# Optimization experiments

Measured on AMD Instinct MI355X. Metric: run time of the kernel, lower is better.

## Reference

```python
import jax, jax.numpy as jnp
import numpy as np

POOL = 4      # pool_size
SR = 2        # sampling_ratio (fixed; torchvision adaptive default approximated)
C_IN = 1024
C1, C2 = 256, 128
OUT_DIM = 2048


def setup_inputs() -> dict:
    key = jax.random.key(0)
    ks = jax.random.split(key, 10)
    B, C, H, W = 8, C_IN, 64, 64
    N = 64
    x = jax.random.normal(ks[0], (B, C, H, W), dtype=jnp.float32)
    # boxes in image pixel coords (image is H*16 = 1024 px)
    img = 1024.0
    x1 = jax.random.uniform(ks[1], (B, N), minval=0.0, maxval=img - 260.0)
    y1 = jax.random.uniform(ks[2], (B, N), minval=0.0, maxval=img - 260.0)
    bw = jax.random.uniform(ks[3], (B, N), minval=32.0, maxval=256.0)
    bh = jax.random.uniform(ks[4], (B, N), minval=32.0, maxval=256.0)
    boxes = jnp.stack([x1, y1, x1 + bw, y1 + bh], axis=-1)  # [B,N,4]
    scale = jnp.float32(1.0 / 16.0)
    # detector params
    w1 = jax.random.normal(ks[5], (C1, C_IN), dtype=jnp.float32) / np.sqrt(C_IN)
    b1 = jnp.zeros((C1,), dtype=jnp.float32)
    w2 = jax.random.normal(ks[6], (C2, C1), dtype=jnp.float32) / np.sqrt(C1)
    b2 = jnp.zeros((C2,), dtype=jnp.float32)
    wl = jax.random.normal(ks[7], (OUT_DIM, C2 * POOL * POOL), dtype=jnp.float32) / np.sqrt(C2 * POOL * POOL)
    bl = jnp.zeros((OUT_DIM,), dtype=jnp.float32)
    return {"x": x, "boxes": boxes, "scale": scale,
            "w1": w1, "b1": b1, "w2": w2, "b2": b2, "wl": wl, "bl": bl}


def _axis_coords(start, size, H):
    # start,size: [R]; returns coords [R, POOL*SR], valid mask, int low/high, lerp wts
    bin_sz = size / POOL                       # [R]
    j = jnp.arange(POOL * SR, dtype=jnp.float32)
    off = jnp.floor(j / SR) + ((j % SR) + 0.5) / SR   # [P]
    c = start[:, None] + off[None, :] * bin_sz[:, None]  # [R,P]
    valid = (c >= -1.0) & (c <= H)
    c = jnp.clip(c, 0.0, H - 1.0)
    lo = jnp.floor(c).astype(jnp.int32)
    lo = jnp.minimum(lo, H - 1)
    hi = jnp.minimum(lo + 1, H - 1)
    frac = c - lo.astype(c.dtype)
    return valid, lo, hi, frac


def _roi_align(feat, boxes, scale):
    # feat: [B,C,H,W], boxes: [B,N,4] -> pooled [B*N, C, POOL, POOL]
    B, C, H, W = feat.shape
    N = boxes.shape[1]
    R = B * N
    bx = (boxes.reshape(R, 4) * scale)
    x1, y1, x2, y2 = bx[:, 0], bx[:, 1], bx[:, 2], bx[:, 3]
    rw = jnp.maximum(x2 - x1, 1.0)
    rh = jnp.maximum(y2 - y1, 1.0)
    vy, y_lo, y_hi, ly = _axis_coords(y1, rh, H)   # [R,P]
    vx, x_lo, x_hi, lx = _axis_coords(x1, rw, W)
    hy, hx = 1.0 - ly, 1.0 - lx
    bidx = jnp.repeat(jnp.arange(B, dtype=jnp.int32), N)  # [R]
    b = bidx[:, None, None]
    # gather 4 corners -> [R,P,P,C]
    v00 = feat[b, :, y_lo[:, :, None], x_lo[:, None, :]]
    v01 = feat[b, :, y_lo[:, :, None], x_hi[:, None, :]]
    v10 = feat[b, :, y_hi[:, :, None], x_lo[:, None, :]]
    v11 = feat[b, :, y_hi[:, :, None], x_hi[:, None, :]]
    w00 = (hy[:, :, None] * hx[:, None, :])[..., None]
    w01 = (hy[:, :, None] * lx[:, None, :])[..., None]
    w10 = (ly[:, :, None] * hx[:, None, :])[..., None]
    w11 = (ly[:, :, None] * lx[:, None, :])[..., None]
    val = v00 * w00 + v01 * w01 + v10 * w10 + v11 * w11
    mask = (vy[:, :, None] & vx[:, None, :])[..., None]
    val = jnp.where(mask, val, 0.0)            # [R,P,P,C]
    val = val.reshape(R, POOL, SR, POOL, SR, C).mean(axis=(2, 4))  # [R,POOL,POOL,C]
    return jnp.transpose(val, (0, 3, 1, 2))    # [R,C,POOL,POOL]


def reference(x, boxes, scale, w1, b1, w2, b2, wl, bl):
    pooled = _roi_align(x, boxes, scale)                  # [R,C,4,4]
    h = jax.nn.elu(jnp.einsum('rchw,oc->rohw', pooled, w1) + b1[None, :, None, None])
    h = jax.nn.elu(jnp.einsum('rchw,oc->rohw', h, w2) + b2[None, :, None, None])
    h = h.reshape(h.shape[0], -1)                         # [R, 128*16], torch Flatten order
    out = jax.nn.elu(h @ wl.T + bl)                       # [R, 2048]
    return out
```

## Files before the change

kernel.cpp:

```cpp
#include <hip/hip_runtime.h>
#include <math.h>

#define C_INK   1024
#define C1D     256
#define C2D     128
#define OUTD    2048
#define R_ROI   512
#define MPIX    32768

#define NSIDE   128

typedef _Float16 half8 __attribute__((ext_vector_type(8)));
typedef float    f32x4 __attribute__((ext_vector_type(4)));

__device__ __forceinline__ unsigned int pack2h(float a, float b) {
    union { _Float16 h[2]; unsigned int u; } p;
    p.h[0] = (_Float16)a; p.h[1] = (_Float16)b;
    return p.u;
}
__device__ __forceinline__ float eluf(float v) { return v > 0.f ? v : expf(v) - 1.f; }

template<int RC>
__device__ __forceinline__ half8* ldsq(_Float16* base, int row, int ch) {
    return reinterpret_cast<half8*>(base) + row * RC + (ch ^ (row & 7));
}

__global__ __launch_bounds__(256) void cvt_w1(
    const float* __restrict__ w1, _Float16* __restrict__ w1h)
{
    const int i0 = (blockIdx.x * 256 + threadIdx.x) * 4;
    #pragma unroll
    for (int j = 0; j < 4; ++j) {
        const int i = (i0 + j) * 4;
        const float4 v = *reinterpret_cast<const float4*>(w1 + i);
        uint2 u; u.x = pack2h(v.x, v.y); u.y = pack2h(v.z, v.w);
        *reinterpret_cast<uint2*>(w1h + i) = u;
    }
}

__global__ __launch_bounds__(512, 4) void conv1x1_f16(
    const float* __restrict__ x, const _Float16* __restrict__ w1h,
    const float* __restrict__ w2, const float* __restrict__ wl,
    _Float16* __restrict__ w2h, _Float16* __restrict__ wlh,
    _Float16* __restrict__ z)
{
    const int bid = blockIdx.x;
    const int tid = threadIdx.x;

    if (bid < NSIDE) {
        constexpr int NF4_W2 = (C2D * C1D) / 4;
        constexpr int NF4    = NF4_W2 + (OUTD * OUTD) / 4;
        for (int i = bid * 512 + tid; i < NF4; i += NSIDE * 512) {
            const float* s; _Float16* d; int e;
            if (i < NF4_W2) { s = w2; d = w2h; e = i * 4; }
            else            { s = wl; d = wlh; e = (i - NF4_W2) * 4; }
            const float4 v = *reinterpret_cast<const float4*>(s + e);
            uint2 u; u.x = pack2h(v.x, v.y); u.y = pack2h(v.z, v.w);
            *reinterpret_cast<uint2*>(d + e) = u;
        }
        return;
    }

    __shared__ __align__(16) _Float16 As[2][64 * 64];

    const int lane = tid & 63;
    const int wave = tid >> 6;
    const int m0   = (bid - NSIDE) * 64;
    const int b    = m0 >> 12;
    const int p0   = m0 & 4095;

    const float* xbase = x + (size_t)b * C_INK * 4096 + p0 + lane;
    const _Float16* wbase = w1h + (size_t)(wave * 32 + (lane & 15)) * C_INK + (lane >> 4) * 8;

    float ar_a[8], ar_b[8];
    half8 bf_a[2][2], bf_b[2][2];
    f32x4 acc[4][2];
    #pragma unroll
    for (int i = 0; i < 4; ++i)
        #pragma unroll
        for (int j = 0; j < 2; ++j) acc[i][j] = (f32x4){0.f, 0.f, 0.f, 0.f};

    auto LOADA = [&](float (&ar)[8], int k0) {
        const float* xk = xbase + (size_t)(k0 + wave * 8) * 4096;
        #pragma unroll
        for (int j = 0; j < 8; ++j) ar[j] = xk[(size_t)j * 4096];
    };
    auto LOADB = [&](half8 (&bf)[2][2], int k0) {
        #pragma unroll
        for (int kk = 0; kk < 2; ++kk)
            #pragma unroll
            for (int ni = 0; ni < 2; ++ni)
                bf[kk][ni] = *reinterpret_cast<const half8*>(
                    wbase + (size_t)ni * 16 * C_INK + k0 + kk * 32);
    };
    auto WRITEA = [&](int buf, float (&ar)[8]) {
        union { half8 h; unsigned int u[4]; } pk;
        #pragma unroll
        for (int j = 0; j < 4; ++j) pk.u[j] = pack2h(ar[2 * j], ar[2 * j + 1]);
        *ldsq<8>(&As[buf][0], lane, wave) = pk.h;
    };
    auto COMPUTE = [&](int buf, half8 (&bf)[2][2]) {
        #pragma unroll
        for (int kk = 0; kk < 2; ++kk) {
            const int ch = kk * 4 + (lane >> 4);
            half8 af[4];
            #pragma unroll
            for (int mi = 0; mi < 4; ++mi)
                af[mi] = *ldsq<8>(&As[buf][0], mi * 16 + (lane & 15), ch);
            #pragma unroll
            for (int mi = 0; mi < 4; ++mi)
                #pragma unroll
                for (int ni = 0; ni < 2; ++ni)
                    acc[mi][ni] = __builtin_amdgcn_mfma_f32_16x16x32_f16(bf[kk][ni], af[mi], acc[mi][ni], 0, 0, 0);
        }
    };

    LOADA(ar_a, 0);   LOADB(bf_a, 0);
    LOADA(ar_b, 64);  LOADB(bf_b, 64);
    WRITEA(0, ar_a);
    __syncthreads();

    #pragma unroll
    for (int tp = 0; tp < 8; ++tp) {
        const int t = 2 * tp;
        if (tp < 7) LOADA(ar_a, (t + 2) * 64);
        WRITEA(1, ar_b);
        COMPUTE(0, bf_a);
        if (tp < 7) LOADB(bf_a, (t + 2) * 64);
        __syncthreads();
        if (tp < 7) {
            LOADA(ar_b, (t + 3) * 64);
            WRITEA(0, ar_a);
        }
        COMPUTE(1, bf_b);
        if (tp < 7) LOADB(bf_b, (t + 3) * 64);
        __syncthreads();
    }

    _Float16* zp = z + (size_t)m0 * C1D;
    #pragma unroll
    for (int mi = 0; mi < 4; ++mi) {
        const int pixel = mi * 16 + (lane & 15);
        #pragma unroll
        for (int ni = 0; ni < 2; ++ni) {
            const int oc0 = wave * 32 + ni * 16 + (lane >> 4) * 4;
            uint2 u;
            u.x = pack2h(acc[mi][ni][0], acc[mi][ni][1]);
            u.y = pack2h(acc[mi][ni][2], acc[mi][ni][3]);
            *reinterpret_cast<uint2*>(&zp[(size_t)pixel * C1D + oc0]) = u;
        }
    }
}

__global__ __launch_bounds__(512) void roi_gemm2_f16(
    const _Float16* __restrict__ z, const float* __restrict__ boxes,
    const float* __restrict__ scale_p, const float* __restrict__ b1v,
    const _Float16* __restrict__ w2h, const float* __restrict__ b2v,
    _Float16* __restrict__ h2)
{
    __shared__ __align__(16) _Float16 H1s[16 * 256];
    __shared__ int   s_off[64][4];
    __shared__ float s_w[64][4];

    const int bid  = blockIdx.x;
    const int r    = (bid & 7) * 64 + (bid >> 3);
    const int tid  = threadIdx.x;
    const int lane = tid & 63;
    const int wv   = tid >> 6;

    half8 bfr[8];
    {
        const _Float16* wp = w2h + (size_t)(wv * 16 + (lane & 15)) * C1D + (lane >> 4) * 8;
        #pragma unroll
        for (int ks = 0; ks < 8; ++ks)
            bfr[ks] = *reinterpret_cast<const half8*>(wp + ks * 32);
    }

    if (tid < 64) {
        const float sc = scale_p[0];
        const float x1 = boxes[r * 4 + 0] * sc, y1 = boxes[r * 4 + 1] * sc;
        const float x2 = boxes[r * 4 + 2] * sc, y2 = boxes[r * 4 + 3] * sc;
        const float rw = fmaxf(x2 - x1, 1.f), rh = fmaxf(y2 - y1, 1.f);
        const int jy = tid >> 3, jx = tid & 7;

        float offy = (float)(jy >> 1) + (float)(jy & 1) * 0.5f + 0.25f;
        float cy = y1 + offy * rh * 0.25f;
        const bool vy = (cy >= -1.f) && (cy <= 64.f);
        cy = fminf(fmaxf(cy, 0.f), 63.f);
        int ylo = (int)cy; if (ylo > 63) ylo = 63;
        int yhi = ylo + 1; if (yhi > 63) yhi = 63;
        const float ly = cy - (float)ylo, hy = 1.f - ly;

        float offx = (float)(jx >> 1) + (float)(jx & 1) * 0.5f + 0.25f;
        float cx = x1 + offx * rw * 0.25f;
        const bool vx = (cx >= -1.f) && (cx <= 64.f);
        cx = fminf(fmaxf(cx, 0.f), 63.f);
        int xlo = (int)cx; if (xlo > 63) xlo = 63;
        int xhi = xlo + 1; if (xhi > 63) xhi = 63;
        const float lx = cx - (float)xlo, hx = 1.f - lx;

        const float wm = (vy && vx) ? 0.25f : 0.f;
        s_w[tid][0] = hy * hx * wm;
        s_w[tid][1] = hy * lx * wm;
        s_w[tid][2] = ly * hx * wm;
        s_w[tid][3] = ly * lx * wm;
        s_off[tid][0] = (ylo * 64 + xlo) * C1D;
        s_off[tid][1] = (ylo * 64 + xhi) * C1D;
        s_off[tid][2] = (yhi * 64 + xlo) * C1D;
        s_off[tid][3] = (yhi * 64 + xhi) * C1D;
    }
    __syncthreads();

    {
        const int ch8  = tid & 31;
        const int cell = tid >> 5;
        const _Float16* zb = z + (size_t)(r >> 6) * 4096 * C1D + ch8 * 8;

        float accv[8];
        #pragma unroll
        for (int e = 0; e < 8; ++e) accv[e] = 0.f;

        const int py = cell >> 2, px = cell & 3;
        #pragma unroll
        for (int u = 0; u < 4; ++u) {
            const int s = (py * 2 + (u >> 1)) * 8 + px * 2 + (u & 1);
            #pragma unroll
            for (int k = 0; k < 4; ++k) {
                const half8 v = *reinterpret_cast<const half8*>(zb + s_off[s][k]);
                const float w = s_w[s][k];
                #pragma unroll
                for (int e = 0; e < 8; ++e) accv[e] += (float)v[e] * w;
            }
        }

        const float4 b0 = *reinterpret_cast<const float4*>(&b1v[ch8 * 8]);
        const float4 b4 = *reinterpret_cast<const float4*>(&b1v[ch8 * 8 + 4]);
        half8 o;
        o[0] = (_Float16)eluf(accv[0] + b0.x); o[1] = (_Float16)eluf(accv[1] + b0.y);
        o[2] = (_Float16)eluf(accv[2] + b0.z); o[3] = (_Float16)eluf(accv[3] + b0.w);
        o[4] = (_Float16)eluf(accv[4] + b4.x); o[5] = (_Float16)eluf(accv[5] + b4.y);
        o[6] = (_Float16)eluf(accv[6] + b4.z); o[7] = (_Float16)eluf(accv[7] + b4.w);
        *ldsq<32>(H1s, cell, ch8) = o;
    }
    __syncthreads();

    f32x4 oa = (f32x4){0.f, 0.f, 0.f, 0.f};
    #pragma unroll
    for (int ks = 0; ks < 8; ++ks) {
        const int ch = ks * 4 + (lane >> 4);
        const half8 af = *ldsq<32>(H1s, lane & 15, ch);
        oa = __builtin_amdgcn_mfma_f32_16x16x32_f16(af, bfr[ks], oa, 0, 0, 0);
    }

    {
        const int o  = wv * 16 + (lane & 15);
        const int p0 = (lane >> 4) * 4;
        const float bv = b2v[o];
        uint2 u;
        u.x = pack2h(eluf(oa[0] + bv), eluf(oa[1] + bv));
        u.y = pack2h(eluf(oa[2] + bv), eluf(oa[3] + bv));
        *reinterpret_cast<uint2*>(&h2[(size_t)r * 2048 + o * 16 + p0]) = u;
    }
}

__global__ __launch_bounds__(512) void gemm_nt_out(
    const _Float16* __restrict__ A, const _Float16* __restrict__ W,
    const float* __restrict__ bias, float* __restrict__ Cout)
{
    constexpr int K = OUTD, N = OUTD;
    __shared__ __align__(16) _Float16 As[64 * 128];
    __shared__ __align__(16) _Float16 Bs[64 * 128];

    const int bid  = blockIdx.x;
    const int m0   = (bid >> 5) * 64;
    const int n0   = (bid & 31) * 64;

    const int tid  = threadIdx.x;
    const int lane = tid & 63;
    const int wave = tid >> 6;
    const int wr   = wave >> 2, wc = wave & 3;
    const int c    = tid & 7;
    const int r0   = tid >> 3;

    half8 arg[2], brg[2];
    f32x4 acc[2];
    acc[0] = (f32x4){0.f, 0.f, 0.f, 0.f};
    acc[1] = (f32x4){0.f, 0.f, 0.f, 0.f};

    auto LOADT = [&](int k0) {
        const _Float16* ap = &A[(size_t)(m0 + r0) * K + k0 + c * 16];
        arg[0] = *reinterpret_cast<const half8*>(ap);
        arg[1] = *reinterpret_cast<const half8*>(ap + 8);
        const _Float16* wp = &W[(size_t)(n0 + r0) * K + k0 + c * 16];
        brg[0] = *reinterpret_cast<const half8*>(wp);
        brg[1] = *reinterpret_cast<const half8*>(wp + 8);
    };
    auto WRITET = [&]() {
        *ldsq<16>(As, r0, 2 * c)     = arg[0];
        *ldsq<16>(As, r0, 2 * c + 1) = arg[1];
        *ldsq<16>(Bs, r0, 2 * c)     = brg[0];
        *ldsq<16>(Bs, r0, 2 * c + 1) = brg[1];
    };
    auto COMPUTET = [&]() {
        #pragma unroll
        for (int kk = 0; kk < 4; ++kk) {
            const int ch = kk * 4 + (lane >> 4);
            half8 af[2], bf;
            af[0] = *ldsq<16>(As, wr * 32 + (lane & 15), ch);
            af[1] = *ldsq<16>(As, wr * 32 + 16 + (lane & 15), ch);
            bf    = *ldsq<16>(Bs, wc * 16 + (lane & 15), ch);
            acc[0] = __builtin_amdgcn_mfma_f32_16x16x32_f16(bf, af[0], acc[0], 0, 0, 0);
            acc[1] = __builtin_amdgcn_mfma_f32_16x16x32_f16(bf, af[1], acc[1], 0, 0, 0);
        }
    };

    constexpr int nt = K / 128;
    LOADT(0); WRITET(); __syncthreads();
    for (int t = 0; t < nt - 1; ++t) {
        LOADT((t + 1) * 128);
        COMPUTET();
        __syncthreads();
        WRITET();
        __syncthreads();
    }
    COMPUTET();

    #pragma unroll
    for (int mi = 0; mi < 2; ++mi) {
        const int row  = m0 + wr * 32 + mi * 16 + (lane & 15);
        const int col0 = n0 + wc * 16 + (lane >> 4) * 4;
        const float4 bv = *reinterpret_cast<const float4*>(&bias[col0]);
        float4 o;
        o.x = eluf(acc[mi][0] + bv.x);
        o.y = eluf(acc[mi][1] + bv.y);
        o.z = eluf(acc[mi][2] + bv.z);
        o.w = eluf(acc[mi][3] + bv.w);
        *reinterpret_cast<float4*>(&Cout[(size_t)row * N + col0]) = o;
    }
}

extern "C" void kernel_launch(void* const* d_in, const int* in_sizes, int n_in,
                              void* d_out, int out_size, void* d_ws, size_t ws_size,
                              hipStream_t stream) {
    const float* x     = (const float*)d_in[0];
    const float* boxes = (const float*)d_in[1];
    const float* scale = (const float*)d_in[2];
    const float* w1    = (const float*)d_in[3];
    const float* b1    = (const float*)d_in[4];
    const float* w2    = (const float*)d_in[5];
    const float* b2    = (const float*)d_in[6];
    const float* wl    = (const float*)d_in[7];
    const float* bl    = (const float*)d_in[8];
    float* out = (float*)d_out;

    _Float16* z   = (_Float16*)d_ws;
    _Float16* h2  = z   + (size_t)MPIX * C1D;
    _Float16* w1h = h2  + (size_t)R_ROI * OUTD;
    _Float16* w2h = w1h + (size_t)C1D * C_INK;
    _Float16* wlh = w2h + (size_t)C2D * C1D;

    cvt_w1<<<dim3(64), dim3(256), 0, stream>>>(w1, w1h);

    conv1x1_f16<<<dim3(NSIDE + MPIX / 64), dim3(512), 0, stream>>>(
        x, w1h, w2, wl, w2h, wlh, z);

    roi_gemm2_f16<<<dim3(R_ROI), dim3(512), 0, stream>>>(
        z, boxes, scale, b1, w2h, b2, h2);

    gemm_nt_out<<<dim3(256), dim3(512), 0, stream>>>(h2, wlh, bl, out);
}
```

Before: 77.47 us.

## Halve conv1x1 pixel tile to 32 and raise occupancy to 8 blocks

Shrinks the conv1x1 tile from 64 to 32 pixels per block, which doubles the grid and raises the launch-bounds occupancy hint from 4 to 8. Weight fragments are now loaded from global memory inside each compute step instead of being prefetched one stage ahead, and the LDS write layout changes so two k-rows share a lane group. The aim is more waves in flight to hide the latency of the strided x loads. In exchange, the w1 weights are re-read twice as often across blocks, and weight-load latency is no longer overlapped by the software pipeline.

New measurement: 107.3 us. +38.5%, slower.

```diff
diff --git a/kernel.cpp b/kernel.cpp
--- a/kernel.cpp
+++ b/kernel.cpp
@@ -38,7 +38,7 @@
     }
 }
 
-__global__ __launch_bounds__(512, 4) void conv1x1_f16(
+__global__ __launch_bounds__(512, 8) void conv1x1_f16(
     const float* __restrict__ x, const _Float16* __restrict__ w1h,
     const float* __restrict__ w2, const float* __restrict__ wl,
     _Float16* __restrict__ w2h, _Float16* __restrict__ wlh,
@@ -61,85 +61,78 @@
         return;
     }
 
-    __shared__ __align__(16) _Float16 As[2][64 * 64];
+    __shared__ __align__(16) _Float16 As[2][32 * 64];
 
     const int lane = tid & 63;
     const int wave = tid >> 6;
-    const int m0   = (bid - NSIDE) * 64;
+    const int m0   = (bid - NSIDE) * 32;
     const int b    = m0 >> 12;
     const int p0   = m0 & 4095;
-
-    const float* xbase = x + (size_t)b * C_INK * 4096 + p0 + lane;
+    const int px   = lane & 31;
+    const int krow = lane >> 5;
+
+    const float* xbase = x + (size_t)b * C_INK * 4096 + p0 + px;
     const _Float16* wbase = w1h + (size_t)(wave * 32 + (lane & 15)) * C_INK + (lane >> 4) * 8;
 
-    float ar_a[8], ar_b[8];
-    half8 bf_a[2][2], bf_b[2][2];
-    f32x4 acc[4][2];
-    #pragma unroll
-    for (int i = 0; i < 4; ++i)
+    float ar_a[4], ar_b[4];
+    f32x4 acc[2][2];
+    #pragma unroll
+    for (int i = 0; i < 2; ++i)
         #pragma unroll
         for (int j = 0; j < 2; ++j) acc[i][j] = (f32x4){0.f, 0.f, 0.f, 0.f};
 
-    auto LOADA = [&](float (&ar)[8], int k0) {
-        const float* xk = xbase + (size_t)(k0 + wave * 8) * 4096;
-        #pragma unroll
-        for (int j = 0; j < 8; ++j) ar[j] = xk[(size_t)j * 4096];
-    };
-    auto LOADB = [&](half8 (&bf)[2][2], int k0) {
+    auto LOADA = [&](float (&ar)[4], int t) {
+        const float* xk = xbase + (size_t)(t * 64 + wave * 8 + krow * 4) * 4096;
+        #pragma unroll
+        for (int j = 0; j < 4; ++j) ar[j] = xk[(size_t)j * 4096];
+    };
+    auto WRITEA = [&](int buf, float (&ar)[4]) {
+        uint2 u; u.x = pack2h(ar[0], ar[1]); u.y = pack2h(ar[2], ar[3]);
+        char* p = (char*)&As[buf][0] + px * 128 + ((wave ^ (px & 7)) << 4) + krow * 8;
+        *reinterpret_cast<uint2*>(p) = u;
+    };
+    auto COMPUTE = [&](int buf, int t) {
+        half8 bf[2][2];
         #pragma unroll
         for (int kk = 0; kk < 2; ++kk)
             #pragma unroll
             for (int ni = 0; ni < 2; ++ni)
                 bf[kk][ni] = *reinterpret_cast<const half8*>(
-                    wbase + (size_t)ni * 16 * C_INK + k0 + kk * 32);
-    };
-    auto WRITEA = [&](int buf, float (&ar)[8]) {
-        union { half8 h; unsigned int u[4]; } pk;
-        #pragma unroll
-        for (int j = 0; j < 4; ++j) pk.u[j] = pack2h(ar[2 * j], ar[2 * j + 1]);
-        *ldsq<8>(&As[buf][0], lane, wave) = pk.h;
-    };
-    auto COMPUTE = [&](int buf, half8 (&bf)[2][2]) {
+                    wbase + (size_t)ni * 16 * C_INK + t * 64 + kk * 32);
         #pragma unroll
         for (int kk = 0; kk < 2; ++kk) {
             const int ch = kk * 4 + (lane >> 4);
-            half8 af[4];
+            half8 af[2];
             #pragma unroll
-            for (int mi = 0; mi < 4; ++mi)
+            for (int mi = 0; mi < 2; ++mi)
                 af[mi] = *ldsq<8>(&As[buf][0], mi * 16 + (lane & 15), ch);
             #pragma unroll
-            for (int mi = 0; mi < 4; ++mi)
+            for (int mi = 0; mi < 2; ++mi)
                 #pragma unroll
                 for (int ni = 0; ni < 2; ++ni)
                     acc[mi][ni] = __builtin_amdgcn_mfma_f32_16x16x32_f16(bf[kk][ni], af[mi], acc[mi][ni], 0, 0, 0);
         }
     };
 
-    LOADA(ar_a, 0);   LOADB(bf_a, 0);
-    LOADA(ar_b, 64);  LOADB(bf_b, 64);
-    WRITEA(0, ar_a);
+    LOADA(ar_a, 0); WRITEA(0, ar_a);
+    LOADA(ar_b, 1);
     __syncthreads();
 
     #pragma unroll
     for (int tp = 0; tp < 8; ++tp) {
         const int t = 2 * tp;
-        if (tp < 7) LOADA(ar_a, (t + 2) * 64);
         WRITEA(1, ar_b);
-        COMPUTE(0, bf_a);
-        if (tp < 7) LOADB(bf_a, (t + 2) * 64);
+        if (tp < 7) LOADA(ar_a, t + 2);
+        COMPUTE(0, t);
         __syncthreads();
-        if (tp < 7) {
-            LOADA(ar_b, (t + 3) * 64);
-            WRITEA(0, ar_a);
-        }
-        COMPUTE(1, bf_b);
-        if (tp < 7) LOADB(bf_b, (t + 3) * 64);
+        if (tp < 7) { WRITEA(0, ar_a); LOADA(ar_b, t + 3); }
+        COMPUTE(1, t + 1);
         __syncthreads();
     }
 
     _Float16* zp = z + (size_t)m0 * C1D;
     #pragma unroll
-    for (int mi = 0; mi < 4; ++mi) {
+    for (int mi = 0; mi < 2; ++mi) {
         const int pixel = mi * 16 + (lane & 15);
         #pragma unroll
         for (int ni = 0; ni < 2; ++ni) {
@@ -361,7 +354,7 @@
 
     cvt_w1<<<dim3(64), dim3(256), 0, stream>>>(w1, w1h);
 
-    conv1x1_f16<<<dim3(NSIDE + MPIX / 64), dim3(512), 0, stream>>>(
+    conv1x1_f16<<<dim3(NSIDE + MPIX / 32), dim3(512), 0, stream>>>(
         x, w1h, w2, wl, w2h, wlh, z);
 
     roi_gemm2_f16<<<dim3(R_ROI), dim3(512), 0, stream>>>(
```
